# Optimization experiments

Hardware: AMD Instinct MI355X
Metric: run time of the kernel (lower is better)

The kernel has to match this reference:

```python
import jax, jax.numpy as jnp
import numpy as np

B, N, K = 4, 100000, 128
Q_MIN = 0.5
S_B = 1.0
POT_SCALE = 1.0
REP_SCALE = 1.0
BETA_SCALE = 1.0
E_WEIGHT = 1.0
POS_WEIGHT = 1.0
TIME_WEIGHT = 1.0
HUBER_D = 2.0


def setup_inputs() -> dict:
    key = jax.random.key(0)
    ks = jax.random.split(key, 9)
    return {
        "beta": jax.random.uniform(ks[0], (B, N), dtype=jnp.float32),
        "ccoords": jax.random.normal(ks[1], (B, N, 2), dtype=jnp.float32),
        "pred_energy": jax.random.uniform(ks[2], (B, N), dtype=jnp.float32),
        "pred_pos": jax.random.normal(ks[3], (B, N, 2), dtype=jnp.float32),
        "pred_time": jax.random.uniform(ks[4], (B, N), dtype=jnp.float32),
        "t_energy": jax.random.uniform(ks[5], (B, N), dtype=jnp.float32),
        "t_pos": jax.random.normal(ks[6], (B, N, 2), dtype=jnp.float32),
        "t_time": jax.random.uniform(ks[7], (B, N), dtype=jnp.float32),
        "t_idx": jax.random.randint(ks[8], (B, N), 0, K + 1, dtype=jnp.int32),
    }


def _huber(x, d):
    a = jnp.abs(x)
    return jnp.where(a <= d, 0.5 * x * x, d * (a - 0.5 * d))


def _oc_loss(beta, ccoords, pred_energy, pred_pos, pred_time,
             t_energy, t_pos, t_time, t_idx):
    eps = 1e-4
    beta = jnp.clip(beta, eps, 1.0 - eps)
    q = jnp.arctanh(beta) ** 2 + Q_MIN                     # [B,N]

    obj = t_idx - 1                                        # -1 = noise, 0..K-1 = object id
    M = obj[:, :, None] == jnp.arange(K, dtype=jnp.int32)  # [B,N,K] bool membership
    Mf = M.astype(q.dtype)
    obj_exists = jnp.any(M, axis=1)                        # [B,K]
    exf = obj_exists.astype(q.dtype)

    # condensation point per object = member hit with max charge q (segment argmax)
    q_masked = jnp.where(M, q[:, :, None], -1.0)           # [B,N,K]
    alpha = jnp.argmax(q_masked, axis=1)                   # [B,K]
    x_alpha = jnp.take_along_axis(ccoords, alpha[:, :, None], axis=1)  # [B,K,2]
    q_alpha = jnp.take_along_axis(q, alpha, axis=1)        # [B,K]
    beta_alpha = jnp.take_along_axis(beta, alpha, axis=1)  # [B,K]

    # pairwise hit <-> condensation-point distances, [B,N,K]
    diff = ccoords[:, :, None, :] - x_alpha[:, None, :, :]
    dist = jnp.sqrt(jnp.sum(diff * diff, axis=-1) + 1e-12)

    qq = q[:, :, None] * q_alpha[:, None, :] * exf[:, None, :]
    v_att = qq * (dist * dist) * Mf
    v_rep = qq * jax.nn.relu(1.0 - dist) * (1.0 - Mf)
    n_tot = jnp.asarray(B * N, q.dtype)
    L_att = jnp.sum(v_att) / n_tot
    L_rep = jnp.sum(v_rep) / n_tot

    # beta loss: pull condensation-point betas to 1, suppress noise betas
    n_obj = jnp.maximum(jnp.sum(exf), 1.0)
    L_beta_obj = jnp.sum((1.0 - beta_alpha) * exf) / n_obj
    noise = (t_idx == 0).astype(q.dtype)
    L_noise = jnp.sum(beta * noise) / jnp.maximum(jnp.sum(noise), 1.0)
    L_beta = L_beta_obj + S_B * L_noise

    # payload losses, beta-weighted over non-noise hits
    p = (jnp.arctanh(beta) ** 2) * (1.0 - noise)           # [B,N]
    p_sum = jnp.maximum(jnp.sum(p), 1e-6)
    L_energy = jnp.sum(p * _huber(pred_energy - t_energy, HUBER_D)) / p_sum
    L_pos = jnp.sum(p * jnp.sum((pred_pos - t_pos) ** 2, axis=-1)) / p_sum
    L_time = jnp.sum(p * (pred_time - t_time) ** 2) / p_sum

    return (POT_SCALE * L_att + REP_SCALE * L_rep + BETA_SCALE * L_beta
            + E_WEIGHT * L_energy + POS_WEIGHT * L_pos + TIME_WEIGHT * L_time)


def reference(beta, ccoords, pred_energy, pred_pos, pred_time,
              t_energy, t_pos, t_time, t_idx):
    return _oc_loss(beta, ccoords, pred_energy, pred_pos, pred_time,
                    t_energy, t_pos, t_time, t_idx)
```

## Files before the change

### kernel.cpp

```cpp
#include <hip/hip_runtime.h>
#include <math.h>

#define BB 4
#define NN 100000
#define KK 128


__device__ __forceinline__ float clipb(float b) {
    return fminf(fmaxf(b, 1e-4f), 1.0f - 1e-4f);
}

__global__ void k_argmax(const float* __restrict__ beta,
                         const int* __restrict__ tidx,
                         unsigned long long* __restrict__ packed) {
    int b = blockIdx.y;
    __shared__ unsigned long long smax[KK];
    for (int t = threadIdx.x; t < KK; t += blockDim.x) smax[t] = 0ULL;
    __syncthreads();
    const float* betab = beta + b * NN;
    const int*   tib   = tidx + b * NN;
    for (int n = blockIdx.x * blockDim.x + threadIdx.x; n < NN;
         n += gridDim.x * blockDim.x) {
        int obj = tib[n] - 1;
        if (obj >= 0) {
            unsigned hi = __float_as_uint(clipb(betab[n]));
            unsigned long long key = ((unsigned long long)hi << 32) |
                                     (unsigned long long)(0xFFFFFFFFu - (unsigned)n);
            atomicMax(&smax[obj], key);
        }
    }
    __syncthreads();
    for (int t = threadIdx.x; t < KK; t += blockDim.x) {
        unsigned long long v = smax[t];
        if (v) atomicMax(&packed[b * KK + t], v);
    }
}

__global__ void k_gather(const unsigned long long* __restrict__ packed,
                         const float2* __restrict__ cc,
                         float4* __restrict__ sobj,
                         float* __restrict__ acc) {
    int t = blockIdx.x * blockDim.x + threadIdx.x;
    if (t >= BB * KK) return;
    int b = t / KK;
    unsigned long long v = packed[t];
    float4 o = make_float4(0.f, 0.f, 0.f, 0.f);
    if (v) {
        unsigned n = 0xFFFFFFFFu - (unsigned)(v & 0xFFFFFFFFu);
        float ba = __uint_as_float((unsigned)(v >> 32));
        float at = atanhf(ba);
        float2 c = cc[b * NN + (int)n];
        o.x = c.x; o.y = c.y; o.z = at * at + 0.5f; o.w = 1.0f;
        atomicAdd(&acc[8], 1.0f);
        atomicAdd(&acc[9], 1.0f - ba);
    }
    sobj[t] = o;
}

#define HH 2

__global__ void __launch_bounds__(256) k_main(
    const float*  __restrict__ beta, const float2* __restrict__ cc,
    const float*  __restrict__ pe,   const float2* __restrict__ pp,
    const float*  __restrict__ pt,   const float*  __restrict__ te,
    const float2* __restrict__ tp,   const float*  __restrict__ tt,
    const int*    __restrict__ tidx, const float4* __restrict__ sobjg,
    float* __restrict__ acc) {
    int b = blockIdx.y;
    __shared__ float4 sobj[KK];
    __shared__ float sred[4][8];
    for (int t = threadIdx.x; t < KK; t += blockDim.x) sobj[t] = sobjg[b * KK + t];
    __syncthreads();

    float p_att = 0.f, p_rep = 0.f, p_nb = 0.f, p_nc = 0.f;
    float p_ps = 0.f, p_e = 0.f, p_pos = 0.f, p_tm = 0.f;

    int n0 = blockIdx.x * (256 * HH) + threadIdx.x;
    int n1 = n0 + 256;
    bool v0 = n0 < NN, v1 = n1 < NN;
    int i0 = b * NN + (v0 ? n0 : 0);
    int i1 = b * NN + (v1 ? n1 : 0);

    float2 c0 = cc[i0], c1 = cc[i1];
    float rep0 = 0.f, rep1 = 0.f;

    #pragma unroll 8
    for (int k = 0; k < KK; ++k) {
        float4 o = sobj[k];
        float dx0 = c0.x - o.x, dy0 = c0.y - o.y;
        float dx1 = c1.x - o.x, dy1 = c1.y - o.y;
        float s0 = fmaf(dx0, dx0, fmaf(dy0, dy0, 1e-12f));
        float s1 = fmaf(dx1, dx1, fmaf(dy1, dy1, 1e-12f));
        float d0 = sqrtf(s0), d1 = sqrtf(s1);
        rep0 = fmaf(o.z, fmaxf(1.0f - d0, 0.0f), rep0);
        rep1 = fmaf(o.z, fmaxf(1.0f - d1, 0.0f), rep1);
    }

    #pragma unroll
    for (int h = 0; h < HH; ++h) {
        bool  vld = h ? v1 : v0;
        int   idx = h ? i1 : i0;
        float rep = h ? rep1 : rep0;
        float2 c  = h ? c1 : c0;
        if (!vld) continue;

        float bc  = clipb(beta[idx]);
        float at  = atanhf(bc);
        float at2 = at * at;
        float q   = at2 + 0.5f;
        int   ti  = tidx[idx];
        int   obj = ti - 1;

        if (obj >= 0) {
            float4 o = sobj[obj];
            float dx = c.x - o.x, dy = c.y - o.y;
            float s = fmaf(dx, dx, fmaf(dy, dy, 1e-12f));
            float d = sqrtf(s);
            rep   -= o.z * fmaxf(1.0f - d, 0.0f);
            p_att += q * (o.z * s);
        }
        p_rep += q * rep;

        if (ti == 0) {
            p_nb += bc;
            p_nc += 1.0f;
        } else {
            p_ps += at2;
            float de = pe[idx] - te[idx];
            float a  = fabsf(de);
            float hb = (a <= 2.0f) ? (0.5f * de * de) : (2.0f * (a - 1.0f));
            p_e  += at2 * hb;
            float2 ppv = pp[idx], tpv = tp[idx];
            float dpx = ppv.x - tpv.x, dpy = ppv.y - tpv.y;
            p_pos += at2 * (dpx * dpx + dpy * dpy);
            float dt = pt[idx] - tt[idx];
            p_tm += at2 * dt * dt;
        }
    }

    float vals[8] = {p_att, p_rep, p_nb, p_nc, p_ps, p_e, p_pos, p_tm};
    int lane = threadIdx.x & 63, wave = threadIdx.x >> 6;
    #pragma unroll
    for (int i = 0; i < 8; ++i) {
        float v = vals[i];
        for (int off = 32; off > 0; off >>= 1) v += __shfl_down(v, off, 64);
        if (lane == 0) sred[wave][i] = v;
    }
    __syncthreads();
    if (threadIdx.x < 8) {
        float s = sred[0][threadIdx.x] + sred[1][threadIdx.x] +
                  sred[2][threadIdx.x] + sred[3][threadIdx.x];
        atomicAdd(&acc[threadIdx.x], s);
    }
}

__global__ void k_final(const float* __restrict__ acc, float* __restrict__ out) {
    float inv_n  = 1.0f / (float)(BB * NN);
    float L_att  = acc[0] * inv_n;
    float L_rep  = acc[1] * inv_n;
    float n_obj  = fmaxf(acc[8], 1.0f);
    float L_beta = acc[9] / n_obj + acc[2] / fmaxf(acc[3], 1.0f);
    float p_sum  = fmaxf(acc[4], 1e-6f);
    out[0] = L_att + L_rep + L_beta + (acc[5] + acc[6] + acc[7]) / p_sum;
}

extern "C" void kernel_launch(void* const* d_in, const int* in_sizes, int n_in,
                              void* d_out, int out_size, void* d_ws, size_t ws_size,
                              hipStream_t stream) {
    const float*  beta = (const float*)d_in[0];
    const float2* cc   = (const float2*)d_in[1];
    const float*  pe   = (const float*)d_in[2];
    const float2* pp   = (const float2*)d_in[3];
    const float*  pt   = (const float*)d_in[4];
    const float*  te   = (const float*)d_in[5];
    const float2* tp   = (const float2*)d_in[6];
    const float*  tt   = (const float*)d_in[7];
    const int*    ti   = (const int*)d_in[8];

    unsigned long long* packed = (unsigned long long*)d_ws;
    float4* sobj = (float4*)((char*)d_ws + 4096);
    float*  acc  = (float*)((char*)d_ws + 12288);
    float*  out  = (float*)d_out;

    hipMemsetAsync(d_ws, 0, 12352, stream);

    k_argmax<<<dim3(64, BB), 256, 0, stream>>>(beta, ti, packed);
    k_gather<<<dim3(2), 256, 0, stream>>>(packed, cc, sobj, acc);
    k_main<<<dim3((NN + 256 * HH - 1) / (256 * HH), BB), 256, 0, stream>>>(
        beta, cc, pe, pp, pt, te, tp, tt, ti, sobj, acc);
    k_final<<<1, 1, 0, stream>>>(acc, out);
}
```

Before: 131.1 us.

## Use single-wave blocks with four hits per thread and raw sqrt

The main kernel now runs 64-thread blocks, one wavefront each, and every thread handles four hits instead of two. Each shared-memory object load is reused across four distance computations. The sqrt call becomes the hardware builtin, and the block reduction becomes a wave-only xor shuffle with no shared memory or barrier. This cuts LDS traffic per FLOP and sync overhead, but it raises register pressure and increases the number of global atomics, since there is one set per wave instead of one per 256 threads.

Measured after the change: 128.5 us. 1.02x faster.

```diff
diff --git a/kernel.cpp b/kernel.cpp
--- a/kernel.cpp
+++ b/kernel.cpp
@@ -4,6 +4,8 @@
 #define BB 4
 #define NN 100000
 #define KK 128
+#define HB 64
+#define HH 4
 
 
 __device__ __forceinline__ float clipb(float b) {
@@ -57,9 +59,7 @@
     sobj[t] = o;
 }
 
-#define HH 2
-
-__global__ void __launch_bounds__(256) k_main(
+__global__ void __launch_bounds__(HB) k_main(
     const float*  __restrict__ beta, const float2* __restrict__ cc,
     const float*  __restrict__ pe,   const float2* __restrict__ pp,
     const float*  __restrict__ pt,   const float*  __restrict__ te,
@@ -68,41 +68,41 @@
     float* __restrict__ acc) {
     int b = blockIdx.y;
     __shared__ float4 sobj[KK];
-    __shared__ float sred[4][8];
-    for (int t = threadIdx.x; t < KK; t += blockDim.x) sobj[t] = sobjg[b * KK + t];
+    for (int t = threadIdx.x; t < KK; t += HB) sobj[t] = sobjg[b * KK + t];
     __syncthreads();
+
+    int base = blockIdx.x * (HB * HH) + threadIdx.x;
+    int   nn[HH]; bool vv[HH]; int ii[HH];
+    float2 ch[HH]; float rp[HH];
+    #pragma unroll
+    for (int h = 0; h < HH; ++h) {
+        nn[h] = base + h * HB;
+        vv[h] = nn[h] < NN;
+        ii[h] = b * NN + (vv[h] ? nn[h] : 0);
+        ch[h] = cc[ii[h]];
+        rp[h] = 0.f;
+    }
+
+    #pragma unroll 4
+    for (int k = 0; k < KK; ++k) {
+        float4 o = sobj[k];
+        #pragma unroll
+        for (int h = 0; h < HH; ++h) {
+            float dx = ch[h].x - o.x, dy = ch[h].y - o.y;
+            float s  = fmaf(dx, dx, fmaf(dy, dy, 1e-12f));
+            float d  = __builtin_amdgcn_sqrtf(s);
+            rp[h] = fmaf(o.z, fmaxf(1.0f - d, 0.0f), rp[h]);
+        }
+    }
 
     float p_att = 0.f, p_rep = 0.f, p_nb = 0.f, p_nc = 0.f;
     float p_ps = 0.f, p_e = 0.f, p_pos = 0.f, p_tm = 0.f;
 
-    int n0 = blockIdx.x * (256 * HH) + threadIdx.x;
-    int n1 = n0 + 256;
-    bool v0 = n0 < NN, v1 = n1 < NN;
-    int i0 = b * NN + (v0 ? n0 : 0);
-    int i1 = b * NN + (v1 ? n1 : 0);
-
-    float2 c0 = cc[i0], c1 = cc[i1];
-    float rep0 = 0.f, rep1 = 0.f;
-
-    #pragma unroll 8
-    for (int k = 0; k < KK; ++k) {
-        float4 o = sobj[k];
-        float dx0 = c0.x - o.x, dy0 = c0.y - o.y;
-        float dx1 = c1.x - o.x, dy1 = c1.y - o.y;
-        float s0 = fmaf(dx0, dx0, fmaf(dy0, dy0, 1e-12f));
-        float s1 = fmaf(dx1, dx1, fmaf(dy1, dy1, 1e-12f));
-        float d0 = sqrtf(s0), d1 = sqrtf(s1);
-        rep0 = fmaf(o.z, fmaxf(1.0f - d0, 0.0f), rep0);
-        rep1 = fmaf(o.z, fmaxf(1.0f - d1, 0.0f), rep1);
-    }
-
     #pragma unroll
     for (int h = 0; h < HH; ++h) {
-        bool  vld = h ? v1 : v0;
-        int   idx = h ? i1 : i0;
-        float rep = h ? rep1 : rep0;
-        float2 c  = h ? c1 : c0;
-        if (!vld) continue;
+        if (!vv[h]) continue;
+        int idx = ii[h];
+        float rep = rp[h];
 
         float bc  = clipb(beta[idx]);
         float at  = atanhf(bc);
@@ -113,9 +113,9 @@
 
         if (obj >= 0) {
             float4 o = sobj[obj];
-            float dx = c.x - o.x, dy = c.y - o.y;
+            float dx = ch[h].x - o.x, dy = ch[h].y - o.y;
             float s = fmaf(dx, dx, fmaf(dy, dy, 1e-12f));
-            float d = sqrtf(s);
+            float d = __builtin_amdgcn_sqrtf(s);
             rep   -= o.z * fmaxf(1.0f - d, 0.0f);
             p_att += q * (o.z * s);
         }
@@ -139,19 +139,16 @@
     }
 
     float vals[8] = {p_att, p_rep, p_nb, p_nc, p_ps, p_e, p_pos, p_tm};
-    int lane = threadIdx.x & 63, wave = threadIdx.x >> 6;
+    int lane = threadIdx.x & 63;
+    float mine = 0.f;
     #pragma unroll
     for (int i = 0; i < 8; ++i) {
         float v = vals[i];
-        for (int off = 32; off > 0; off >>= 1) v += __shfl_down(v, off, 64);
-        if (lane == 0) sred[wave][i] = v;
+        #pragma unroll
+        for (int off = 32; off > 0; off >>= 1) v += __shfl_xor(v, off, 64);
+        if (lane == i) mine = v;
     }
-    __syncthreads();
-    if (threadIdx.x < 8) {
-        float s = sred[0][threadIdx.x] + sred[1][threadIdx.x] +
-                  sred[2][threadIdx.x] + sred[3][threadIdx.x];
-        atomicAdd(&acc[threadIdx.x], s);
-    }
+    if (lane < 8) atomicAdd(&acc[lane], mine);
 }
 
 __global__ void k_final(const float* __restrict__ acc, float* __restrict__ out) {
@@ -186,7 +183,7 @@
 
     k_argmax<<<dim3(64, BB), 256, 0, stream>>>(beta, ti, packed);
     k_gather<<<dim3(2), 256, 0, stream>>>(packed, cc, sobj, acc);
-    k_main<<<dim3((NN + 256 * HH - 1) / (256 * HH), BB), 256, 0, stream>>>(
+    k_main<<<dim3((NN + HB * HH - 1) / (HB * HH), BB), HB, 0, stream>>>(
         beta, cc, pe, pp, pt, te, tp, tt, ti, sobj, acc);
     k_final<<<1, 1, 0, stream>>>(acc, out);
 }
```
